# Performance work log

Measured on AMD Instinct MI355X. Metric: run time of the kernel, lower is better.

## Reference

```python
import jax, jax.numpy as jnp
import numpy as np

T, D, E, K = 8192, 7168, 256, 8
G, LG = 8, 4  # n_expert_groups, n_limited_groups
ROUTE_SCALE = 2.5


def setup_inputs() -> dict:
    key = jax.random.key(0)
    k1, k2, k3 = jax.random.split(key, 3)
    x = jax.random.normal(k1, (T, D), dtype=jnp.float32)
    W = jax.random.normal(k2, (E, D), dtype=jnp.float32) * (1.0 / np.sqrt(D))
    bias = jax.random.normal(k3, (E,), dtype=jnp.float32) * 0.01
    return {"x": x, "W": W, "bias": bias}


def reference(x, W, bias):
    # linear scorer: [T, E]
    logits = jnp.einsum("td,ed->te", x, W)
    original_scores = jax.nn.sigmoid(logits)
    scores = original_scores + bias  # bias only affects routing, not weights

    # group selection: reshape [T, G, E//G]; group score = sum of top-2 (bias path)
    scores_g = scores.reshape(T, G, E // G)
    group_scores = jax.lax.top_k(scores_g, 2)[0].sum(axis=-1)  # [T, G]
    _, gidx = jax.lax.top_k(group_scores, LG)  # [T, LG]
    keep = jnp.any(jnp.arange(G)[None, None, :] == gidx[:, :, None], axis=1)  # [T, G]
    scores_masked = jnp.where(keep[:, :, None], scores_g, -jnp.inf).reshape(T, E)

    # final top-k experts
    _, indices = jax.lax.top_k(scores_masked, K)  # [T, K] int32
    weights = jnp.take_along_axis(original_scores, indices, axis=1)  # [T, K]
    weights = weights / weights.sum(axis=-1, keepdims=True)  # sigmoid normalization
    weights = weights * ROUTE_SCALE
    weights = weights.astype(x.dtype)

    # per-expert token counts (indices unique per row, so scatter(1)+sum == histogram)
    counts = jnp.zeros((E,), dtype=jnp.int32).at[indices.reshape(-1)].add(1)
    return weights, indices.astype(jnp.int64), counts
```

## Files before the change

### kernel.cpp

```cpp
#include <hip/hip_runtime.h>
#include <math.h>
#include <stdint.h>

#define T_TOK 8192
#define D_DIM 7168
#define E_EXP 256
#define K_SEL 8
#define G_GRP 8
#define LG_GRP 4
#define ROUTE_SCALE 2.5f

#define BM 64
#define BN 128
#define BK 64
#define NKT (D_DIM / BK)
#define KT_HALF (NKT / 2)
#define SCALE_LO 2048.0f
#define INV_SCALE (1.0f / 2048.0f)

typedef _Float16 half_t;
typedef _Float16 half8 __attribute__((ext_vector_type(8)));
typedef float f32x4 __attribute__((ext_vector_type(4)));

#define WF_HALVES_PER_H (2 * 112 * 16 * 512)

__device__ __forceinline__ void load_lds16(const void* g, void* l) {
    __builtin_amdgcn_global_load_lds(
        (const __attribute__((address_space(1))) uint32_t*)g,
        (__attribute__((address_space(3))) uint32_t*)l, 16, 0, 0);
}

__global__ __launch_bounds__(256)
void convert_W_kernel(const float* __restrict__ W, half_t* __restrict__ Wf) {
    const int u = blockIdx.x * 256 + threadIdx.x;
    const int slot = u & 63;
    const int ks   = (u >> 6) & 1;
    const int p    = (u >> 7) & 7;
    const int t2   = u >> 10;
    const int kt   = t2 % 112;
    const int nb   = t2 / 112;
    const int e = nb * 128 + p * 16 + (slot & 15);
    const int k = kt * 64 + ks * 32 + (slot >> 4) * 8;

    const float* src = W + (size_t)e * D_DIM + k;
    float4 v0 = *(const float4*)src;
    float4 v1 = *(const float4*)(src + 4);
    float f[8] = {v0.x, v0.y, v0.z, v0.w, v1.x, v1.y, v1.z, v1.w};
    half8 hi, lo;
    #pragma unroll
    for (int j = 0; j < 8; j++) {
        const half_t h = (half_t)f[j];
        hi[j] = h;
        lo[j] = (half_t)((f[j] - (float)h) * SCALE_LO);
    }
    *(half8*)&Wf[(size_t)u * 8] = hi;
    *(half8*)&Wf[(size_t)WF_HALVES_PER_H + (size_t)u * 8] = lo;
}

__global__ __launch_bounds__(256, 2)
void gemm_logits_f16split(const float* __restrict__ x,
                          const half_t* __restrict__ Wf,
                          float* __restrict__ plane0,
                          float* __restrict__ plane1) {
    __shared__ __align__(16) half_t Ah[4 * 2 * 64 * 8];
    __shared__ __align__(16) half_t Al[4 * 2 * 64 * 8];
    __shared__ __align__(16) half_t Bbuf[2][32][512];

    const int tid = threadIdx.x;
    const int bid = blockIdx.x;
    const int nb    = bid & 1;
    const int split = (bid >> 1) & 1;
    const int m_blk = bid >> 2;
    const int row0 = m_blk * BM;
    const int ks0  = split * KT_HALF;

    const float* __restrict__ xA = x + (size_t)row0 * D_DIM;
    float* __restrict__ plane = split ? plane1 : plane0;

    const int wave = tid >> 6, lane = tid & 63;
    const int q = lane >> 4;
    const int mp0 = (wave >> 1) * 2;
    const int np0 = (wave & 1) * 4;

    float4 pa[2][2];

    auto load_A = [&](int kt) {
        const int kbase = kt * BK;
        #pragma unroll
        for (int i = 0; i < 2; i++) {
            const int u = i * 256 + tid;
            const int r = u >> 3, k8 = u & 7;
            const float* p = xA + (size_t)r * D_DIM + kbase + k8 * 8;
            pa[i][0] = *(const float4*)p;
            pa[i][1] = *(const float4*)(p + 4);
        }
    };

    auto stage_A = [&]() {
        #pragma unroll
        for (int i = 0; i < 2; i++) {
            const int u = i * 256 + tid;
            const int r = u >> 3, k8 = u & 7;
            float f[8] = {pa[i][0].x, pa[i][0].y, pa[i][0].z, pa[i][0].w,
                          pa[i][1].x, pa[i][1].y, pa[i][1].z, pa[i][1].w};
            half8 hi, lo;
            #pragma unroll
            for (int j = 0; j < 8; j++) {
                const half_t h = (half_t)f[j];
                hi[j] = h;
                lo[j] = (half_t)((f[j] - (float)h) * SCALE_LO);
            }
            const int m = r & 15, qq = k8 & 3, kss = k8 >> 2;
            const int slot = (m + 16 * qq) ^ k8;
            const int off = (((r >> 4) * 2 + kss) * 64 + slot) * 8;
            *(half8*)&Ah[off] = hi;
            *(half8*)&Al[off] = lo;
        }
    };

    auto issue_B = [&](int tt) {
        const int kt = ks0 + tt;
        half_t* bb = &Bbuf[tt & 1][0][0];
        #pragma unroll
        for (int i = 0; i < 8; i++) {
            const int s32 = i * 4 + wave;
            const int h = s32 >> 4, sl = s32 & 15;
            const half_t* src = Wf +
                ((size_t)((h * 2 + nb) * 112 + kt) * 16 + sl) * 512 + lane * 8;
            load_lds16(src, bb + s32 * 512);
        }
    };

    f32x4 ach[2][4] = {}, acc[2][4] = {};

    auto compute = [&](int tt) {
        const half_t* bb = &Bbuf[tt & 1][0][0];
        #pragma unroll
        for (int ks = 0; ks < 2; ks++) {
            const int slot = lane ^ ((ks << 2) | q);
            half8 ah[2], al[2], bh[4], bl[4];
            #pragma unroll
            for (int mi = 0; mi < 2; mi++) {
                const int off = (((mp0 + mi) * 2 + ks) * 64 + slot) * 8;
                ah[mi] = *(const half8*)&Ah[off];
                al[mi] = *(const half8*)&Al[off];
            }
            #pragma unroll
            for (int ni = 0; ni < 4; ni++) {
                const int s32 = (np0 + ni) * 2 + ks;
                bh[ni] = *(const half8*)&bb[s32 * 512 + lane * 8];
                bl[ni] = *(const half8*)&bb[(16 + s32) * 512 + lane * 8];
            }
            #pragma unroll
            for (int mi = 0; mi < 2; mi++)
                #pragma unroll
                for (int ni = 0; ni < 4; ni++) {
                    ach[mi][ni] = __builtin_amdgcn_mfma_f32_16x16x32_f16(ah[mi], bh[ni], ach[mi][ni], 0, 0, 0);
                    acc[mi][ni] = __builtin_amdgcn_mfma_f32_16x16x32_f16(ah[mi], bl[ni], acc[mi][ni], 0, 0, 0);
                    acc[mi][ni] = __builtin_amdgcn_mfma_f32_16x16x32_f16(al[mi], bh[ni], acc[mi][ni], 0, 0, 0);
                }
        }
    };

    issue_B(0);
    load_A(ks0);

    #pragma unroll 1
    for (int tt = 0; tt < KT_HALF; tt++) {
        __syncthreads();
        stage_A();
        __syncthreads();
        if (tt + 1 < KT_HALF) {
            issue_B(tt + 1);
            load_A(ks0 + tt + 1);
        }
        compute(tt);
    }

    const int col0 = nb * BN;
    #pragma unroll
    for (int mi = 0; mi < 2; mi++)
        #pragma unroll
        for (int ni = 0; ni < 4; ni++) {
            const f32x4 vh = ach[mi][ni];
            const f32x4 vc = acc[mi][ni];
            const int ex = col0 + (np0 + ni) * 16 + (lane & 15);
            #pragma unroll
            for (int r = 0; r < 4; r++) {
                const int tok = row0 + (mp0 + mi) * 16 + q * 4 + r;
                plane[(size_t)tok * E_EXP + ex] = vh[r] + vc[r] * INV_SCALE;
            }
        }
}

__global__ __launch_bounds__(256)
void routing_kernel(const float* __restrict__ plane0,
                    const float* __restrict__ plane1,
                    const float* __restrict__ bias,
                    float* __restrict__ out_w,
                    float* __restrict__ out_i) {
    const int wave = threadIdx.x >> 6;
    const int lane = threadIdx.x & 63;
    const int t    = blockIdx.x * 4 + wave;

    const float4 l0 = *(const float4*)(plane0 + (size_t)t * E_EXP + lane * 4);
    const float4 l1 = *(const float4*)(plane1 + (size_t)t * E_EXP + lane * 4);
    const float4 bi = *(const float4*)(bias + lane * 4);
    float lg[4] = {l0.x + l1.x, l0.y + l1.y, l0.z + l1.z, l0.w + l1.w};

    float orig[4], s[4];
    #pragma unroll
    for (int j = 0; j < 4; j++)
        orig[j] = 1.0f / (1.0f + expf(-lg[j]));
    s[0] = orig[0] + bi.x; s[1] = orig[1] + bi.y;
    s[2] = orig[2] + bi.z; s[3] = orig[3] + bi.w;

    float p1 = fmaxf(s[0], s[1]), p2 = fminf(s[0], s[1]);
    float q1 = fmaxf(s[2], s[3]), q2 = fminf(s[2], s[3]);
    float m1 = fmaxf(p1, q1);
    float m2 = fmaxf(fminf(p1, q1), (p1 >= q1) ? p2 : q2);

    #pragma unroll
    for (int off = 1; off <= 4; off <<= 1) {
        float o1 = __shfl_xor(m1, off);
        float o2 = __shfl_xor(m2, off);
        float M1 = fmaxf(m1, o1);
        float M2 = fmaxf(fminf(m1, o1), (m1 >= o1) ? m2 : o2);
        m1 = M1; m2 = M2;
    }
    const float gscore = m1 + m2;

    const int g = lane >> 3;
    int cnt = 0;
    #pragma unroll
    for (int j = 0; j < G_GRP; j++) {
        float gj = __shfl(gscore, j * 8);
        cnt += (gj > gscore || (gj == gscore && j < g)) ? 1 : 0;
    }
    const bool keep = (cnt < LG_GRP);

    float smask[4];
    #pragma unroll
    for (int j = 0; j < 4; j++) smask[j] = keep ? s[j] : -INFINITY;

    float wsum = 0.0f, my_o = 0.0f;
    int my_i = 0;

    #pragma unroll
    for (int k = 0; k < K_SEL; k++) {
        float bv = smask[0]; float bo = orig[0]; int bs = 0;
        if (smask[1] > bv) { bv = smask[1]; bo = orig[1]; bs = 1; }
        if (smask[2] > bv) { bv = smask[2]; bo = orig[2]; bs = 2; }
        if (smask[3] > bv) { bv = smask[3]; bo = orig[3]; bs = 3; }
        int bidx = lane * 4 + bs;

        #pragma unroll
        for (int off = 32; off >= 1; off >>= 1) {
            float ov = __shfl_xor(bv, off);
            float oo = __shfl_xor(bo, off);
            int   oi = __shfl_xor(bidx, off);
            if (ov > bv || (ov == bv && oi < bidx)) { bv = ov; bo = oo; bidx = oi; }
        }
        wsum += bo;
        if (lane == k) { my_o = bo; my_i = bidx; }
        if ((bidx >> 2) == lane) {
            const int sl = bidx & 3;
            smask[0] = (sl == 0) ? -INFINITY : smask[0];
            smask[1] = (sl == 1) ? -INFINITY : smask[1];
            smask[2] = (sl == 2) ? -INFINITY : smask[2];
            smask[3] = (sl == 3) ? -INFINITY : smask[3];
        }
    }

    if (lane < K_SEL) {
        out_w[(size_t)t * K_SEL + lane] = my_o * ROUTE_SCALE / wsum;
        out_i[(size_t)t * K_SEL + lane] = (float)my_i;
    }
}

__global__ __launch_bounds__(256)
void count_kernel(const float* __restrict__ idxf, float* __restrict__ out_c) {
    const float fe = (float)blockIdx.x;
    int c = 0;
    const float4* p = (const float4*)idxf;
    for (int i = threadIdx.x; i < (T_TOK * K_SEL / 4); i += 256) {
        float4 v = p[i];
        c += (v.x == fe) + (v.y == fe) + (v.z == fe) + (v.w == fe);
    }
    __shared__ int red[4];
    #pragma unroll
    for (int off = 32; off >= 1; off >>= 1) c += __shfl_down(c, off);
    if ((threadIdx.x & 63) == 0) red[threadIdx.x >> 6] = c;
    __syncthreads();
    if (threadIdx.x == 0)
        out_c[blockIdx.x] = (float)(red[0] + red[1] + red[2] + red[3]);
}

extern "C" void kernel_launch(void* const* d_in, const int* in_sizes, int n_in,
                              void* d_out, int out_size, void* d_ws, size_t ws_size,
                              hipStream_t stream) {
    const float* x    = (const float*)d_in[0];
    const float* W    = (const float*)d_in[1];
    const float* bias = (const float*)d_in[2];

    float* out   = (float*)d_out;
    float* out_w = out;
    float* out_i = out + (size_t)T_TOK * K_SEL;
    float* out_c = out + (size_t)2 * T_TOK * K_SEL;

    float* plane0 = (float*)d_ws;
    float* plane1 = plane0 + (size_t)T_TOK * E_EXP;
    half_t* Wf    = (half_t*)(plane1 + (size_t)T_TOK * E_EXP);

    hipLaunchKernelGGL(convert_W_kernel, dim3(896), dim3(256), 0, stream, W, Wf);
    hipLaunchKernelGGL(gemm_logits_f16split, dim3(512), dim3(256), 0, stream,
                       x, Wf, plane0, plane1);
    hipLaunchKernelGGL(routing_kernel, dim3(T_TOK / 4), dim3(256), 0, stream,
                       plane0, plane1, bias, out_w, out_i);
    hipLaunchKernelGGL(count_kernel, dim3(E_EXP), dim3(256), 0, stream,
                       out_i, out_c);
}
```

Measured before the change: 393.6 us.

## Double GEMM M-tile to 128 rows and hoist A conversion before barrier

Raises the GEMM M-tile from 64 to 128 tokens. Each 4-wave block now computes a 4x4 grid of MFMA tiles per wave and reuses every W tile loaded into LDS across twice as many rows, which halves the W traffic. The grid drops to 256 blocks with a remapped block index, and launch bounds go to 1 block per SM. The fp32-to-f16 split conversion of A now runs before the first barrier so it can overlap the wait. The cost is fewer resident waves (lower occupancy), higher register pressure from 32 accumulators, and only 256 blocks across the CUs.

```diff
diff --git a/kernel.cpp b/kernel.cpp
--- a/kernel.cpp
+++ b/kernel.cpp
@@ -10,7 +10,7 @@
 #define LG_GRP 4
 #define ROUTE_SCALE 2.5f
 
-#define BM 64
+#define BM 128
 #define BN 128
 #define BK 64
 #define NKT (D_DIM / BK)
@@ -57,20 +57,22 @@
     *(half8*)&Wf[(size_t)WF_HALVES_PER_H + (size_t)u * 8] = lo;
 }
 
-__global__ __launch_bounds__(256, 2)
+__global__ __launch_bounds__(256, 1)
 void gemm_logits_f16split(const float* __restrict__ x,
                           const half_t* __restrict__ Wf,
                           float* __restrict__ plane0,
                           float* __restrict__ plane1) {
-    __shared__ __align__(16) half_t Ah[4 * 2 * 64 * 8];
-    __shared__ __align__(16) half_t Al[4 * 2 * 64 * 8];
+    __shared__ __align__(16) half_t Ah[8 * 2 * 64 * 8];
+    __shared__ __align__(16) half_t Al[8 * 2 * 64 * 8];
     __shared__ __align__(16) half_t Bbuf[2][32][512];
 
     const int tid = threadIdx.x;
     const int bid = blockIdx.x;
-    const int nb    = bid & 1;
-    const int split = (bid >> 1) & 1;
-    const int m_blk = bid >> 2;
+    const int g     = bid & 7;
+    const int j     = bid >> 3;
+    const int nb    = g & 1;
+    const int split = (g >> 1) & 1;
+    const int m_blk = ((g >> 2) << 5) + j;
     const int row0 = m_blk * BM;
     const int ks0  = split * KT_HALF;
 
@@ -79,15 +81,16 @@
 
     const int wave = tid >> 6, lane = tid & 63;
     const int q = lane >> 4;
-    const int mp0 = (wave >> 1) * 2;
+    const int mp0 = (wave >> 1) * 4;
     const int np0 = (wave & 1) * 4;
 
-    float4 pa[2][2];
+    float4 pa[4][2];
+    half8 hreg[4], lreg[4];
 
     auto load_A = [&](int kt) {
         const int kbase = kt * BK;
         #pragma unroll
-        for (int i = 0; i < 2; i++) {
+        for (int i = 0; i < 4; i++) {
             const int u = i * 256 + tid;
             const int r = u >> 3, k8 = u & 7;
             const float* p = xA + (size_t)r * D_DIM + kbase + k8 * 8;
@@ -96,25 +99,30 @@
         }
     };
 
-    auto stage_A = [&]() {
-        #pragma unroll
-        for (int i = 0; i < 2; i++) {
+    auto convert_A = [&]() {
+        #pragma unroll
+        for (int i = 0; i < 4; i++) {
+            float f[8] = {pa[i][0].x, pa[i][0].y, pa[i][0].z, pa[i][0].w,
+                          pa[i][1].x, pa[i][1].y, pa[i][1].z, pa[i][1].w};
+            #pragma unroll
+            for (int jj = 0; jj < 8; jj++) {
+                const half_t h = (half_t)f[jj];
+                hreg[i][jj] = h;
+                lreg[i][jj] = (half_t)((f[jj] - (float)h) * SCALE_LO);
+            }
+        }
+    };
+
+    auto write_A = [&]() {
+        #pragma unroll
+        for (int i = 0; i < 4; i++) {
             const int u = i * 256 + tid;
             const int r = u >> 3, k8 = u & 7;
-            float f[8] = {pa[i][0].x, pa[i][0].y, pa[i][0].z, pa[i][0].w,
-                          pa[i][1].x, pa[i][1].y, pa[i][1].z, pa[i][1].w};
-            half8 hi, lo;
-            #pragma unroll
-            for (int j = 0; j < 8; j++) {
-                const half_t h = (half_t)f[j];
-                hi[j] = h;
-                lo[j] = (half_t)((f[j] - (float)h) * SCALE_LO);
-            }
             const int m = r & 15, qq = k8 & 3, kss = k8 >> 2;
             const int slot = (m + 16 * qq) ^ k8;
             const int off = (((r >> 4) * 2 + kss) * 64 + slot) * 8;
-            *(half8*)&Ah[off] = hi;
-            *(half8*)&Al[off] = lo;
+            *(half8*)&Ah[off] = hreg[i];
+            *(half8*)&Al[off] = lreg[i];
         }
     };
 
@@ -131,16 +139,16 @@
         }
     };
 
-    f32x4 ach[2][4] = {}, acc[2][4] = {};
+    f32x4 ach[4][4] = {}, acc[4][4] = {};
 
     auto compute = [&](int tt) {
         const half_t* bb = &Bbuf[tt & 1][0][0];
         #pragma unroll
         for (int ks = 0; ks < 2; ks++) {
             const int slot = lane ^ ((ks << 2) | q);
-            half8 ah[2], al[2], bh[4], bl[4];
-            #pragma unroll
-            for (int mi = 0; mi < 2; mi++) {
+            half8 ah[4], al[4], bh[4], bl[4];
+            #pragma unroll
+            for (int mi = 0; mi < 4; mi++) {
                 const int off = (((mp0 + mi) * 2 + ks) * 64 + slot) * 8;
                 ah[mi] = *(const half8*)&Ah[off];
                 al[mi] = *(const half8*)&Al[off];
@@ -152,7 +160,7 @@
                 bl[ni] = *(const half8*)&bb[(16 + s32) * 512 + lane * 8];
             }
             #pragma unroll
-            for (int mi = 0; mi < 2; mi++)
+            for (int mi = 0; mi < 4; mi++)
                 #pragma unroll
                 for (int ni = 0; ni < 4; ni++) {
                     ach[mi][ni] = __builtin_amdgcn_mfma_f32_16x16x32_f16(ah[mi], bh[ni], ach[mi][ni], 0, 0, 0);
@@ -167,8 +175,9 @@
 
     #pragma unroll 1
     for (int tt = 0; tt < KT_HALF; tt++) {
+        convert_A();
         __syncthreads();
-        stage_A();
+        write_A();
         __syncthreads();
         if (tt + 1 < KT_HALF) {
             issue_B(tt + 1);
@@ -179,7 +188,7 @@
 
     const int col0 = nb * BN;
     #pragma unroll
-    for (int mi = 0; mi < 2; mi++)
+    for (int mi = 0; mi < 4; mi++)
         #pragma unroll
         for (int ni = 0; ni < 4; ni++) {
             const f32x4 vh = ach[mi][ni];
@@ -313,7 +322,7 @@
     half_t* Wf    = (half_t*)(plane1 + (size_t)T_TOK * E_EXP);
 
     hipLaunchKernelGGL(convert_W_kernel, dim3(896), dim3(256), 0, stream, W, Wf);
-    hipLaunchKernelGGL(gemm_logits_f16split, dim3(512), dim3(256), 0, stream,
+    hipLaunchKernelGGL(gemm_logits_f16split, dim3(256), dim3(256), 0, stream,
                        x, Wf, plane0, plane1);
     hipLaunchKernelGGL(routing_kernel, dim3(T_TOK / 4), dim3(256), 0, stream,
                        plane0, plane1, bias, out_w, out_i);
```

Measured after the change: 435.8 us. 10.7% more time.
